# Kernel optimization log

Hardware: AMD Instinct MI355X
Metric: run time of the kernel (lower is better)

Reference implementation:

```python
import jax, jax.numpy as jnp
import numpy as np
from itertools import product

N = 65536
G = 128          # voxel grid side
K = 27           # 3^3 kernel offsets
C_IN, C_HID, C_OUT = 3, 256, 128
EPS = 1e-5


def _build_neighbors():
    rng = np.random.default_rng(0)
    keys = np.sort(rng.choice(G ** 3, size=N, replace=False))
    coords = np.stack(np.unravel_index(keys, (G, G, G)), axis=-1)  # [N,3]
    offs = np.array(list(product([-1, 0, 1], repeat=3)), dtype=np.int64)  # [27,3]
    nc = coords[:, None, :] + offs[None, :, :]                       # [N,27,3]
    inb = ((nc >= 0) & (nc < G)).all(-1)
    nk = nc[..., 0] * G * G + nc[..., 1] * G + nc[..., 2]
    pos = np.clip(np.searchsorted(keys, np.clip(nk, 0, G ** 3 - 1)), 0, N - 1)
    found = inb & (keys[pos] == nk)
    idx = np.where(found, pos, 0).astype(np.int32)
    return idx, found


def setup_inputs() -> dict:
    key = jax.random.key(0)
    ks = jax.random.split(key, 12)
    idx, mask = _build_neighbors()
    s_in = 1.0 / np.sqrt(K * C_IN)
    s_h = 1.0 / np.sqrt(K * C_HID)
    return {
        "feats": jax.random.normal(ks[0], (N, C_IN), jnp.float32),
        "w_in": jax.random.normal(ks[1], (K, C_IN, C_HID), jnp.float32) * s_in,
        "g_in": jnp.ones((C_HID,), jnp.float32),
        "b_in": jnp.zeros((C_HID,), jnp.float32),
        "w_res": jax.random.normal(ks[2], (4, 2, K, C_HID, C_HID), jnp.float32) * s_h,
        "g_res": jnp.ones((4, 2, C_HID), jnp.float32),
        "b_res": jnp.zeros((4, 2, C_HID), jnp.float32),
        "w_out": jax.random.normal(ks[3], (C_HID, C_OUT), jnp.float32) / np.sqrt(C_HID),
        "nbr_idx": jnp.asarray(idx),
        "nbr_mask": jnp.asarray(mask),
    }


def sparse_conv(feats, W, idx, mask):
    # feats [N,Cin], W [K,Cin,Cout], idx/mask [N,K] -> gather-GEMM-scatter per offset
    def step(acc, xs):
        w_k, i_k, m_k = xs  # [Cin,Cout], [N], [N]
        g = feats[i_k] * m_k[:, None]
        return acc + g @ w_k, None
    init = jnp.zeros((feats.shape[0], W.shape[-1]), feats.dtype)
    out, _ = jax.lax.scan(step, init, (W, idx.T, mask.T.astype(feats.dtype)))
    return out


def bn(x, g, b):
    mu = x.mean(0)
    var = x.var(0)
    return (x - mu) * jax.lax.rsqrt(var + EPS) * g + b


def reference(feats, w_in, g_in, b_in, w_res, g_res, b_res, w_out, nbr_idx, nbr_mask):
    h = jax.nn.relu(bn(sparse_conv(feats, w_in, nbr_idx, nbr_mask), g_in, b_in))
    for i in range(4):  # 4 MinkowskiResBlocks
        r = jax.nn.relu(bn(sparse_conv(h, w_res[i, 0], nbr_idx, nbr_mask), g_res[i, 0], b_res[i, 0]))
        r = bn(sparse_conv(r, w_res[i, 1], nbr_idx, nbr_mask), g_res[i, 1], b_res[i, 1])
        h = jax.nn.relu(r + h)
    return h @ w_out  # kernel_size=1 output conv == pointwise linear
```

## Files before the change

kernel.cpp:

```cpp
#include <hip/hip_runtime.h>
#include <hip/hip_bf16.h>


#define NPTS 65536
#define CHID 256
#define CAP  4096
#define LBLK 256

typedef __bf16 bf16x8 __attribute__((ext_vector_type(8)));
typedef float  f32x4  __attribute__((ext_vector_type(4)));
typedef unsigned short u16x8 __attribute__((ext_vector_type(8)));

__device__ __forceinline__ float bf2f(unsigned short u) {
    union { float f; unsigned v; } x; x.v = ((unsigned)u) << 16; return x.f;
}
__device__ __forceinline__ unsigned short f2bf(float f) {
    union { float f; unsigned v; } x; x.f = f;
    unsigned r = x.v + 0x7fffu + ((x.v >> 16) & 1u);
    return (unsigned short)(r >> 16);
}

__device__ __forceinline__ void gload16(const void* g, void* l) {
    __builtin_amdgcn_global_load_lds(
        (const __attribute__((address_space(1))) void*)g,
        (__attribute__((address_space(3))) void*)l, 16, 0, 0);
}

__device__ __forceinline__ bool mk(const void* mask, int mflag, size_t i) {
    if (mflag) return ((const unsigned char*)mask)[i] != 0;
    return ((const int*)mask)[i] != 0;
}

__global__ void detect_mask(const unsigned char* __restrict__ m, int* __restrict__ flag) {
    int t = blockIdx.x * 256 + threadIdx.x;
    int any = 0;
    for (int i = t; i < 262144; i += 64 * 256)
        if ((i & 3) && m[i]) any = 1;
    if (any) atomicOr(flag, 1);
}

__global__ void pack_w(const float* __restrict__ w, unsigned short* __restrict__ wp) {
    __shared__ float tile[64][65];
    int m   = blockIdx.x;
    int tci = (blockIdx.y >> 2) * 64;
    int tco = (blockIdx.y & 3) * 64;
    const float* src = w + (size_t)m * 65536;
    unsigned short* dst = wp + (size_t)m * 65536;
    int t = threadIdx.x, c = t & 63, rg = t >> 6;
    for (int r = rg; r < 64; r += 4)
        tile[r][c] = src[(size_t)(tci + r) * 256 + tco + c];
    __syncthreads();
    for (int r = rg; r < 64; r += 4)
        dst[(size_t)(tco + r) * 256 + tci + c] = f2bf(tile[c][r]);
}

__global__ void pack_wout(const float* __restrict__ w, unsigned short* __restrict__ wp) {
    __shared__ float tile[64][65];
    int tco = blockIdx.x * 64, tci = blockIdx.y * 64;
    int t = threadIdx.x, c = t & 63, rg = t >> 6;
    for (int r = rg; r < 64; r += 4)
        tile[r][c] = w[(size_t)(tci + r) * 128 + tco + c];
    __syncthreads();
    for (int r = rg; r < 64; r += 4)
        wp[(size_t)(tco + r) * 256 + tci + c] = f2bf(tile[c][r]);
}

__global__ void pack_win(const float* __restrict__ w, unsigned short* __restrict__ wp) {
    __shared__ float tile[64][65];
    int cot = blockIdx.x * 64, kkt = blockIdx.y * 64;
    int t = threadIdx.x, c = t & 63, rg = t >> 6;
    for (int r = rg; r < 64; r += 4) {
        int kk = kkt + r;
        tile[r][c] = (kk < 81) ? w[(size_t)kk * 256 + cot + c] : 0.f;
    }
    __syncthreads();
    for (int r = rg; r < 64; r += 4)
        wp[(size_t)(cot + r) * 128 + kkt + c] = f2bf(tile[c][r]);
}

__global__ void count_lists(const void* __restrict__ mask, const int* __restrict__ mflagp,
                            int* __restrict__ blkcnt ) {
    int mflag = *mflagp;
    int tid = threadIdx.x, lane = tid & 63;
    int n = blockIdx.x * 256 + tid;
    __shared__ int lc[26];
    if (tid < 26) lc[tid] = 0;
    __syncthreads();
    unsigned vb = 0;
    for (int k = 0; k < 27; ++k) {
        if (k == 13) continue;
        if (mk(mask, mflag, (size_t)n * 27 + k)) vb |= 1u << k;
    }
    for (int k26 = 0; k26 < 26; ++k26) {
        int k = (k26 < 13) ? k26 : k26 + 1;
        unsigned long long b = __ballot((vb >> k) & 1);
        if (lane == 0) atomicAdd(&lc[k26], __popcll(b));
    }
    __syncthreads();
    if (tid < 26) blkcnt[tid * LBLK + blockIdx.x] = lc[tid];
}

__global__ void scan_lists(const int* __restrict__ blkcnt, int* __restrict__ bases,
                           int* __restrict__ cnt) {
    int t = threadIdx.x;
    if (t < 26) {
        int s = 0;
        for (int b = 0; b < LBLK; ++b) {
            bases[t * LBLK + b] = s;
            s += blkcnt[t * LBLK + b];
        }
        cnt[t] = s;
    }
}

__global__ void fill_lists(const int* __restrict__ idx, const void* __restrict__ mask,
                           const int* __restrict__ mflagp, const int* __restrict__ bases,
                           int* __restrict__ srcL, int* __restrict__ nbrEnt,
                           unsigned char* __restrict__ nbrCnt) {
    int mflag = *mflagp;
    int tid = threadIdx.x, lane = tid & 63, wave = tid >> 6;
    int n = blockIdx.x * 256 + tid;
    __shared__ int wcnt[4][26];
    unsigned vb = 0;
    for (int k = 0; k < 27; ++k) {
        if (k == 13) continue;
        if (mk(mask, mflag, (size_t)n * 27 + k)) vb |= 1u << k;
    }
    for (int k26 = 0; k26 < 26; ++k26) {
        int k = (k26 < 13) ? k26 : k26 + 1;
        unsigned long long b = __ballot((vb >> k) & 1);
        if (lane == 0) wcnt[wave][k26] = __popcll(b);
    }
    __syncthreads();
    int j = 0;
    for (int k26 = 0; k26 < 26; ++k26) {
        int k = (k26 < 13) ? k26 : k26 + 1;
        bool v = (vb >> k) & 1;
        unsigned long long b = __ballot(v);
        if (v) {
            int p = bases[k26 * LBLK + blockIdx.x] + __popcll(b & ((1ull << lane) - 1ull));
            for (int w = 0; w < wave; ++w) p += wcnt[w][k26];
            if (p < CAP) {
                srcL[k26 * CAP + p] = idx[(size_t)n * 27 + k];
                nbrEnt[n * 32 + j] = k26 * CAP + p;
                ++j;
            }
        }
    }
    nbrCnt[n] = (unsigned char)j;
}

__global__ __launch_bounds__(256, 2)
void convin_gemm(const float* __restrict__ feats, const unsigned short* __restrict__ win,
                 const int* __restrict__ idx, const void* __restrict__ mask,
                 const int* __restrict__ mflagp, unsigned short* __restrict__ yb) {
    __shared__ __align__(16) char A[16384];
    __shared__ __align__(16) char B[32768];
    const int mflag = *mflagp;
    const int tid = threadIdx.x, lane = tid & 63, wave = tid >> 6;
    const int m0 = blockIdx.x * 64;

    for (int i = 0; i < 4; ++i)
        *(f32x4*)&A[tid * 64 + i * 16] = f32x4{0.f, 0.f, 0.f, 0.f};
    __syncthreads();

    {
        int row = tid & 63, g = tid >> 6;
        int n = m0 + row;
        int swz = (row & 7) << 4;
        for (int k = g; k < 27; k += 4) {
            if (mk(mask, mflag, (size_t)n * 27 + k)) {
                int j = idx[(size_t)n * 27 + k];
                float f0 = feats[j * 3 + 0], f1 = feats[j * 3 + 1], f2 = feats[j * 3 + 2];
                int b0 = 2 * (3 * k + 0), b1 = b0 + 2, b2 = b0 + 4;
                *(unsigned short*)&A[row * 256 + (b0 ^ swz)] = f2bf(f0);
                *(unsigned short*)&A[row * 256 + (b1 ^ swz)] = f2bf(f1);
                *(unsigned short*)&A[row * 256 + (b2 ^ swz)] = f2bf(f2);
            }
        }
    }

    const char* wb = (const char*)win;
    f32x4 acc[4][4] = {};

    for (int ks = 0; ks < 2; ++ks) {
        __syncthreads();
        for (int i = 0; i < 8; ++i) {
            int chunk = wave * 8 + i;
            int o = chunk * 1024 + lane * 16;
            int corow = o >> 7;
            int inner = (o & 127) ^ ((corow & 7) << 4);
            gload16(wb + (size_t)corow * 256 + ks * 128 + inner, B + o);
        }
        __syncthreads();
        const int cw = wave * 64;
        for (int kk = 0; kk < 64; kk += 32) {
            int kl = kk + 8 * (lane >> 4);
            bf16x8 af[4], bfr[4];
            for (int mi = 0; mi < 4; ++mi) {
                int row = 16 * mi + (lane & 15);
                af[mi] = *(const bf16x8*)(A + row * 256 + ((ks * 128 + 2 * kl) ^ ((row & 7) << 4)));
            }
            for (int ni = 0; ni < 4; ++ni) {
                int corow = cw + 16 * ni + (lane & 15);
                bfr[ni] = *(const bf16x8*)(B + corow * 128 + ((2 * kl) ^ ((corow & 7) << 4)));
            }
            for (int mi = 0; mi < 4; ++mi)
                for (int ni = 0; ni < 4; ++ni)
                    acc[mi][ni] = __builtin_amdgcn_mfma_f32_16x16x32_bf16(af[mi], bfr[ni], acc[mi][ni], 0, 0, 0);
        }
    }

    const int cw = wave * 64;
    const int rq = 4 * (lane >> 4);
    const int colo = lane & 15;
    for (int mi = 0; mi < 4; ++mi)
        for (int ni = 0; ni < 4; ++ni) {
            int col = cw + 16 * ni + colo;
            for (int r = 0; r < 4; ++r) {
                float v = acc[mi][ni][r];
                float o = __shfl_xor(v, 1);
                if ((lane & 1) == 0) {
                    unsigned pk = (unsigned)f2bf(v) | ((unsigned)f2bf(o) << 16);
                    int row = m0 + 16 * mi + rq + r;
                    *(unsigned*)&yb[(size_t)row * CHID + col] = pk;
                }
            }
        }
}

template<bool GATHER>
__global__ __launch_bounds__(512, 1)
void conv_gemm(const unsigned short* __restrict__ hin,
               const unsigned short* __restrict__ Wp,
               unsigned short* __restrict__ yb,
               const int* __restrict__ cnt,
               const int* __restrict__ srcL) {
    __shared__ __align__(16) char lds[131072];
    __shared__ int ids_src[256];
    const int tid  = threadIdx.x;
    const int lane = tid & 63;
    const int wave = tid >> 6;
    const int wm = wave >> 2;
    const int wn = wave & 3;

    int k27 = 13, m0 = 0, k26 = 0, tile = 0, c = 0;
    if (GATHER) {
        k26 = blockIdx.x;
        k27 = (k26 < 13) ? k26 : k26 + 1;
        tile = blockIdx.y;
        c = min(cnt[k26], CAP);
        if (tile * 256 >= c) return;
        if (tid < 256) {
            int g = tile * 256 + tid;
            ids_src[tid] = (g < c) ? srcL[k26 * CAP + g] : 0;
        }
        __syncthreads();
    } else {
        m0 = blockIdx.x * 256;
    }
    const char* hbase = (const char*)hin;
    const char* wbase = (const char*)(Wp + (size_t)k27 * (CHID * CHID));

    f32x4 acc[8][4] = {};

    auto STAGE = [&](int buf, int ks) {
        const int ci0 = ks * 64;
        char* dst = lds + buf * 65536;
        #pragma unroll
        for (int i = 0; i < 8; ++i) {
            int o = (wave * 8 + i) * 1024 + lane * 16;
            const char* src;
            if (o < 32768) {
                int row = o >> 7;
                int inner = (o & 127) ^ ((row & 7) << 4);
                int grow = GATHER ? ids_src[row] : (m0 + row);
                src = hbase + (size_t)grow * 512 + ci0 * 2 + inner;
            } else {
                int bo = o - 32768;
                int corow = bo >> 7;
                int inner = (bo & 127) ^ ((corow & 7) << 4);
                src = wbase + (size_t)corow * 512 + ci0 * 2 + inner;
            }
            gload16(src, dst + o);
        }
    };

    auto COMPUTE = [&](int buf) {
        const char* A = lds + buf * 65536;
        const char* B = A + 32768;
        #pragma unroll
        for (int kk = 0; kk < 64; kk += 32) {
            int kl = kk + 8 * (lane >> 4);
            bf16x8 af[8], bfr[4];
            #pragma unroll
            for (int mi = 0; mi < 8; ++mi) {
                int row = wm * 128 + 16 * mi + (lane & 15);
                af[mi] = *(const bf16x8*)(A + row * 128 + ((2 * kl) ^ ((row & 7) << 4)));
            }
            #pragma unroll
            for (int ni = 0; ni < 4; ++ni) {
                int corow = wn * 64 + 16 * ni + (lane & 15);
                bfr[ni] = *(const bf16x8*)(B + corow * 128 + ((2 * kl) ^ ((corow & 7) << 4)));
            }
            #pragma unroll
            for (int mi = 0; mi < 8; ++mi)
                #pragma unroll
                for (int ni = 0; ni < 4; ++ni)
                    acc[mi][ni] = __builtin_amdgcn_mfma_f32_16x16x32_bf16(af[mi], bfr[ni], acc[mi][ni], 0, 0, 0);
        }
    };

    STAGE(0, 0);
    __syncthreads();
    int cur = 0;
    #pragma unroll
    for (int ks = 0; ks < 4; ++ks) {
        if (ks < 3) STAGE(cur ^ 1, ks + 1);
        COMPUTE(cur);
        __syncthreads();
        cur ^= 1;
    }

    const int rq = 4 * (lane >> 4);
    const int colo = lane & 15;
    #pragma unroll
    for (int mi = 0; mi < 8; ++mi)
        #pragma unroll
        for (int ni = 0; ni < 4; ++ni) {
            int col = wn * 64 + 16 * ni + colo;
            #pragma unroll
            for (int r = 0; r < 4; ++r) {
                float v = acc[mi][ni][r];
                float o = __shfl_xor(v, 1);
                if ((lane & 1) == 0) {
                    unsigned pk = (unsigned)f2bf(v) | ((unsigned)f2bf(o) << 16);
                    int rl = wm * 128 + 16 * mi + rq + r;
                    if (!GATHER) {
                        *(unsigned*)&yb[(size_t)(m0 + rl) * CHID + col] = pk;
                    } else {
                        int g = tile * 256 + rl;
                        if (g < c)
                            *(unsigned*)&yb[((size_t)k26 * CAP + g) * CHID + col] = pk;
                    }
                }
            }
        }
}

__global__ __launch_bounds__(256)
void combine_stats(unsigned short* __restrict__ Yb,
                   const unsigned short* __restrict__ buf,
                   const int* __restrict__ nbrEnt,
                   const unsigned char* __restrict__ nbrCnt,
                   float* __restrict__ st) {
    __shared__ float ssum[8][256];
    __shared__ float ssq[8][256];
    const int tid = threadIdx.x;
    const int grp = tid >> 5;
    const int c0  = (tid & 31) * 8;
    float s[8] = {}, s2[8] = {};
    const int row0 = blockIdx.x * 128;
    for (int it = 0; it < 16; ++it) {
        int row = row0 + it * 8 + grp;
        size_t off = (size_t)row * CHID + c0;
        u16x8 y = *(const u16x8*)&Yb[off];
        float v[8];
        #pragma unroll
        for (int q = 0; q < 8; ++q) v[q] = bf2f(y[q]);
        int cnt = nbrCnt[row];
        for (int j = 0; j < cnt; ++j) {
            int e = nbrEnt[row * 32 + j];
            u16x8 b = *(const u16x8*)&buf[(size_t)e * CHID + c0];
            #pragma unroll
            for (int q = 0; q < 8; ++q) v[q] += bf2f(b[q]);
        }
        u16x8 o;
        #pragma unroll
        for (int q = 0; q < 8; ++q) {
            o[q] = f2bf(v[q]);
            s[q] += v[q];
            s2[q] += v[q] * v[q];
        }
        *(u16x8*)&Yb[off] = o;
    }
    #pragma unroll
    for (int q = 0; q < 8; ++q) {
        ssum[grp][c0 + q] = s[q];
        ssq[grp][c0 + q]  = s2[q];
    }
    __syncthreads();
    float ts = 0.f, tq = 0.f;
    #pragma unroll
    for (int g = 0; g < 8; ++g) { ts += ssum[g][tid]; tq += ssq[g][tid]; }
    unsafeAtomicAdd(&st[tid], ts);
    unsafeAtomicAdd(&st[256 + tid], tq);
}

__global__ void bn_stats(const unsigned short* __restrict__ yb, float* __restrict__ st) {
    int t = threadIdx.x;
    int b = blockIdx.x;
    float s = 0.f, s2 = 0.f;
    size_t base = (size_t)b * 256 * CHID + t;
    for (int i = 0; i < 256; ++i) {
        float v = bf2f(yb[base + (size_t)i * CHID]);
        s += v; s2 += v * v;
    }
    unsafeAtomicAdd(&st[t], s);
    unsafeAtomicAdd(&st[256 + t], s2);
}

__global__ void bn_apply(const unsigned short* __restrict__ yb, const float* __restrict__ st,
                         const float* __restrict__ g, const float* __restrict__ b,
                         const unsigned short* __restrict__ res, unsigned short* __restrict__ hout) {
    int t = threadIdx.x;
    float mean = st[t] * (1.f / NPTS);
    float var  = st[256 + t] * (1.f / NPTS) - mean * mean;
    float rstd = rsqrtf(var + 1e-5f);
    float sc = rstd * g[t];
    float bi = b[t] - mean * sc;
    size_t row0 = (size_t)blockIdx.x * 32;
    for (int i = 0; i < 32; ++i) {
        size_t off = (row0 + i) * CHID + t;
        float v = bf2f(yb[off]) * sc + bi;
        if (res) v += bf2f(res[off]);
        v = fmaxf(v, 0.f);
        hout[off] = f2bf(v);
    }
}

__global__ __launch_bounds__(256, 2)
void gemm_out(const unsigned short* __restrict__ hin, const unsigned short* __restrict__ wop,
              float* __restrict__ out) {
    __shared__ __align__(16) char lds[16384 + 16384];
    const int tid = threadIdx.x, lane = tid & 63, wave = tid >> 6;
    const int m0 = blockIdx.x * 128;
    const char* hb = (const char*)hin;
    const char* wb = (const char*)wop;
    f32x4 acc[4][4] = {};
    for (int ks = 0; ks < 4; ++ks) {
        int ci0 = ks * 64;
        __syncthreads();
        for (int i = 0; i < 8; ++i) {
            int chunk = wave * 8 + i;
            int o = chunk * 1024 + lane * 16;
            const char* src;
            if (o < 16384) {
                int row = o >> 7;
                int k2 = (o & 127) ^ ((row & 7) << 4);
                src = hb + (size_t)(m0 + row) * 512 + ci0 * 2 + k2;
            } else {
                int bo = o - 16384;
                int corow = bo >> 7;
                int k2 = (bo & 127) ^ ((corow & 7) << 4);
                src = wb + (size_t)corow * 512 + ci0 * 2 + k2;
            }
            gload16(src, lds + chunk * 1024);
        }
        __syncthreads();
        const char* A = lds;
        const char* B = lds + 16384;
        const int wm = wave >> 1, wn = wave & 1;
        for (int kk = 0; kk < 64; kk += 32) {
            int kl = kk + 8 * (lane >> 4);
            bf16x8 af[4], bfr[4];
            for (int mi = 0; mi < 4; ++mi) {
                int row = 64 * wm + 16 * mi + (lane & 15);
                af[mi] = *(const bf16x8*)(A + row * 128 + ((2 * kl) ^ ((row & 7) << 4)));
            }
            for (int ni = 0; ni < 4; ++ni) {
                int corow = 64 * wn + 16 * ni + (lane & 15);
                bfr[ni] = *(const bf16x8*)(B + corow * 128 + ((2 * kl) ^ ((corow & 7) << 4)));
            }
            for (int mi = 0; mi < 4; ++mi)
                for (int ni = 0; ni < 4; ++ni)
                    acc[mi][ni] = __builtin_amdgcn_mfma_f32_16x16x32_bf16(af[mi], bfr[ni], acc[mi][ni], 0, 0, 0);
        }
    }
    const int wm = wave >> 1, wn = wave & 1;
    for (int mi = 0; mi < 4; ++mi)
        for (int ni = 0; ni < 4; ++ni) {
            int col = 64 * wn + 16 * ni + (lane & 15);
            for (int r = 0; r < 4; ++r) {
                int row = m0 + 64 * wm + 16 * mi + 4 * (lane >> 4) + r;
                out[(size_t)row * 128 + col] = acc[mi][ni][r];
            }
        }
}

static const size_t OFF_Y    = 0;
static const size_t OFF_HA   = OFF_Y   + (size_t)NPTS * CHID * 2;
static const size_t OFF_HR   = OFF_HA  + (size_t)NPTS * CHID * 2;
static const size_t OFF_WP   = OFF_HR  + (size_t)NPTS * CHID * 2;
static const size_t OFF_WOP  = OFF_WP  + (size_t)8 * 27 * 65536 * 2;
static const size_t OFF_WIN  = OFF_WOP + (size_t)128 * 256 * 2;
static const size_t OFF_ST   = OFF_WIN + (size_t)256 * 128 * 2;
static const size_t OFF_CNT  = OFF_ST  + 9 * 512 * 4;
static const size_t OFF_FLAG = OFF_CNT + 112;
static const size_t OFF_SRC  = OFF_CNT + 128;
static const size_t OFF_BLK  = OFF_SRC + (size_t)26 * CAP * 4;
static const size_t OFF_BAS  = OFF_BLK + (size_t)26 * LBLK * 4;
static const size_t OFF_NBE  = OFF_BAS + (size_t)26 * LBLK * 4;
static const size_t OFF_NBC  = OFF_NBE + (size_t)NPTS * 32 * 4;
static const size_t OFF_BUF  = OFF_NBC + (size_t)NPTS;

extern "C" void kernel_launch(void* const* d_in, const int* in_sizes, int n_in,
                              void* d_out, int out_size, void* d_ws, size_t ws_size,
                              hipStream_t stream) {
    const float* feats = (const float*)d_in[0];
    const float* w_in  = (const float*)d_in[1];
    const float* g_in  = (const float*)d_in[2];
    const float* b_in  = (const float*)d_in[3];
    const float* w_res = (const float*)d_in[4];
    const float* g_res = (const float*)d_in[5];
    const float* b_res = (const float*)d_in[6];
    const float* w_out = (const float*)d_in[7];
    const int*   nidx  = (const int*)d_in[8];
    const void*  nmask = (const void*)d_in[9];

    char* ws = (char*)d_ws;
    unsigned short* Yb   = (unsigned short*)(ws + OFF_Y);
    unsigned short* HA   = (unsigned short*)(ws + OFF_HA);
    unsigned short* HR   = (unsigned short*)(ws + OFF_HR);
    unsigned short* WP   = (unsigned short*)(ws + OFF_WP);
    unsigned short* WOP  = (unsigned short*)(ws + OFF_WOP);
    unsigned short* WIN  = (unsigned short*)(ws + OFF_WIN);
    float*          ST   = (float*)(ws + OFF_ST);
    int*            CNT  = (int*)(ws + OFF_CNT);
    int*            MFLG = (int*)(ws + OFF_FLAG);
    int*            SRCL = (int*)(ws + OFF_SRC);
    int*            BLKC = (int*)(ws + OFF_BLK);
    int*            BASE = (int*)(ws + OFF_BAS);
    int*            NBE  = (int*)(ws + OFF_NBE);
    unsigned char*  NBC  = (unsigned char*)(ws + OFF_NBC);
    unsigned short* BUF  = (unsigned short*)(ws + OFF_BUF);

    hipMemsetAsync(ws + OFF_ST, 0, 9 * 512 * 4 + 128, stream);

    detect_mask<<<64, 256, 0, stream>>>((const unsigned char*)nmask, MFLG);
    pack_w   <<<dim3(216, 16), 256, 0, stream>>>(w_res, WP);
    pack_wout<<<dim3(2, 4),    256, 0, stream>>>(w_out, WOP);
    pack_win <<<dim3(4, 2),    256, 0, stream>>>(w_in, WIN);

    count_lists<<<LBLK, 256, 0, stream>>>(nmask, MFLG, BLKC);
    scan_lists <<<1, 64, 0, stream>>>(BLKC, BASE, CNT);
    fill_lists <<<LBLK, 256, 0, stream>>>(nidx, nmask, MFLG, BASE, SRCL, NBE, NBC);

    convin_gemm<<<NPTS / 64, 256, 0, stream>>>(feats, WIN, nidx, nmask, MFLG, Yb);
    bn_stats<<<256, 256, 0, stream>>>(Yb, ST);
    bn_apply<<<2048, 256, 0, stream>>>(Yb, ST, g_in, b_in, nullptr, HA);

    for (int c8 = 0; c8 < 8; ++c8) {
        const unsigned short* hin = (c8 & 1) ? HR : HA;
        const unsigned short* wbase = WP + (size_t)c8 * 27 * 65536;
        float* st = ST + (size_t)(1 + c8) * 512;
        conv_gemm<false><<<NPTS / 256, 512, 0, stream>>>(hin, wbase, Yb, nullptr, nullptr);
        conv_gemm<true><<<dim3(26, CAP / 256), 512, 0, stream>>>(hin, wbase, BUF, CNT, SRCL);
        combine_stats<<<512, 256, 0, stream>>>(Yb, BUF, NBE, NBC, st);
        if (c8 & 1) {
            bn_apply<<<2048, 256, 0, stream>>>(Yb, st, g_res + c8 * 256, b_res + c8 * 256, HA, HA);
        } else {
            bn_apply<<<2048, 256, 0, stream>>>(Yb, st, g_res + c8 * 256, b_res + c8 * 256, nullptr, HR);
        }
    }

    gemm_out<<<NPTS / 128, 256, 0, stream>>>(HA, WOP, (float*)d_out);
}
```

Before: 885.4 us.

## Vectorize BN stats/apply and replace atomics with two-stage partial reduction

```diff
diff --git a/kernel.cpp b/kernel.cpp
--- a/kernel.cpp
+++ b/kernel.cpp
@@ -6,6 +6,7 @@
 #define CHID 256
 #define CAP  4096
 #define LBLK 256
+#define CBLK 2048
 
 typedef __bf16 bf16x8 __attribute__((ext_vector_type(8)));
 typedef float  f32x4  __attribute__((ext_vector_type(4)));
@@ -353,15 +354,15 @@
                    const unsigned short* __restrict__ buf,
                    const int* __restrict__ nbrEnt,
                    const unsigned char* __restrict__ nbrCnt,
-                   float* __restrict__ st) {
+                   float* __restrict__ part) {
     __shared__ float ssum[8][256];
     __shared__ float ssq[8][256];
     const int tid = threadIdx.x;
     const int grp = tid >> 5;
     const int c0  = (tid & 31) * 8;
     float s[8] = {}, s2[8] = {};
-    const int row0 = blockIdx.x * 128;
-    for (int it = 0; it < 16; ++it) {
+    const int row0 = blockIdx.x * 32;
+    for (int it = 0; it < 4; ++it) {
         int row = row0 + it * 8 + grp;
         size_t off = (size_t)row * CHID + c0;
         u16x8 y = *(const u16x8*)&Yb[off];
@@ -393,39 +394,88 @@
     float ts = 0.f, tq = 0.f;
     #pragma unroll
     for (int g = 0; g < 8; ++g) { ts += ssum[g][tid]; tq += ssq[g][tid]; }
-    unsafeAtomicAdd(&st[tid], ts);
-    unsafeAtomicAdd(&st[256 + tid], tq);
-}
-
-__global__ void bn_stats(const unsigned short* __restrict__ yb, float* __restrict__ st) {
-    int t = threadIdx.x;
-    int b = blockIdx.x;
-    float s = 0.f, s2 = 0.f;
-    size_t base = (size_t)b * 256 * CHID + t;
-    for (int i = 0; i < 256; ++i) {
-        float v = bf2f(yb[base + (size_t)i * CHID]);
-        s += v; s2 += v * v;
-    }
-    unsafeAtomicAdd(&st[t], s);
-    unsafeAtomicAdd(&st[256 + t], s2);
-}
-
-__global__ void bn_apply(const unsigned short* __restrict__ yb, const float* __restrict__ st,
-                         const float* __restrict__ g, const float* __restrict__ b,
-                         const unsigned short* __restrict__ res, unsigned short* __restrict__ hout) {
-    int t = threadIdx.x;
-    float mean = st[t] * (1.f / NPTS);
-    float var  = st[256 + t] * (1.f / NPTS) - mean * mean;
-    float rstd = rsqrtf(var + 1e-5f);
-    float sc = rstd * g[t];
-    float bi = b[t] - mean * sc;
-    size_t row0 = (size_t)blockIdx.x * 32;
-    for (int i = 0; i < 32; ++i) {
-        size_t off = (row0 + i) * CHID + t;
-        float v = bf2f(yb[off]) * sc + bi;
-        if (res) v += bf2f(res[off]);
-        v = fmaxf(v, 0.f);
-        hout[off] = f2bf(v);
+    part[(size_t)blockIdx.x * 512 + tid]       = ts;
+    part[(size_t)blockIdx.x * 512 + 256 + tid] = tq;
+}
+
+__global__ __launch_bounds__(256)
+void bn_stats_vec(const unsigned short* __restrict__ Yb, float* __restrict__ part) {
+    __shared__ float ssum[8][256];
+    __shared__ float ssq[8][256];
+    const int tid = threadIdx.x;
+    const int grp = tid >> 5;
+    const int c0  = (tid & 31) * 8;
+    float s[8] = {}, s2[8] = {};
+    const int row0 = blockIdx.x * 32;
+    for (int it = 0; it < 4; ++it) {
+        int row = row0 + it * 8 + grp;
+        u16x8 y = *(const u16x8*)&Yb[(size_t)row * CHID + c0];
+        #pragma unroll
+        for (int q = 0; q < 8; ++q) {
+            float v = bf2f(y[q]);
+            s[q] += v; s2[q] += v * v;
+        }
+    }
+    #pragma unroll
+    for (int q = 0; q < 8; ++q) {
+        ssum[grp][c0 + q] = s[q];
+        ssq[grp][c0 + q]  = s2[q];
+    }
+    __syncthreads();
+    float ts = 0.f, tq = 0.f;
+    #pragma unroll
+    for (int g = 0; g < 8; ++g) { ts += ssum[g][tid]; tq += ssq[g][tid]; }
+    part[(size_t)blockIdx.x * 512 + tid]       = ts;
+    part[(size_t)blockIdx.x * 512 + 256 + tid] = tq;
+}
+
+__global__ void reduce_stats(const float* __restrict__ part, float* __restrict__ st) {
+    int gt = blockIdx.x * 256 + threadIdx.x;
+    int c = gt & 511;
+    int chunk = gt >> 9;
+    float s = 0.f;
+    for (int i = 0; i < CBLK / 16; ++i)
+        s += part[(size_t)(chunk * (CBLK / 16) + i) * 512 + c];
+    unsafeAtomicAdd(&st[c], s);
+}
+
+__global__ __launch_bounds__(256)
+void bn_apply(const unsigned short* __restrict__ yb, const float* __restrict__ st,
+              const float* __restrict__ g, const float* __restrict__ b,
+              const unsigned short* __restrict__ res, unsigned short* __restrict__ hout) {
+    const int tid = threadIdx.x;
+    const int grp = tid >> 5;
+    const int c0  = (tid & 31) * 8;
+    float sc[8], bi[8];
+    #pragma unroll
+    for (int q = 0; q < 8; ++q) {
+        float mean = st[c0 + q] * (1.f / NPTS);
+        float var  = st[256 + c0 + q] * (1.f / NPTS) - mean * mean;
+        float rstd = rsqrtf(var + 1e-5f);
+        sc[q] = rstd * g[c0 + q];
+        bi[q] = b[c0 + q] - mean * sc[q];
+    }
+    const int row0 = blockIdx.x * 32;
+    for (int it = 0; it < 4; ++it) {
+        int row = row0 + it * 8 + grp;
+        size_t off = (size_t)row * CHID + c0;
+        u16x8 y = *(const u16x8*)&yb[off];
+        u16x8 o;
+        if (res) {
+            u16x8 rr = *(const u16x8*)&res[off];
+            #pragma unroll
+            for (int q = 0; q < 8; ++q) {
+                float v = bf2f(y[q]) * sc[q] + bi[q] + bf2f(rr[q]);
+                o[q] = f2bf(fmaxf(v, 0.f));
+            }
+        } else {
+            #pragma unroll
+            for (int q = 0; q < 8; ++q) {
+                float v = bf2f(y[q]) * sc[q] + bi[q];
+                o[q] = f2bf(fmaxf(v, 0.f));
+            }
+        }
+        *(u16x8*)&hout[off] = o;
     }
 }
 
@@ -502,7 +552,8 @@
 static const size_t OFF_BAS  = OFF_BLK + (size_t)26 * LBLK * 4;
 static const size_t OFF_NBE  = OFF_BAS + (size_t)26 * LBLK * 4;
 static const size_t OFF_NBC  = OFF_NBE + (size_t)NPTS * 32 * 4;
-static const size_t OFF_BUF  = OFF_NBC + (size_t)NPTS;
+static const size_t OFF_PART = OFF_NBC + (size_t)NPTS;
+static const size_t OFF_BUF  = OFF_PART + (size_t)CBLK * 512 * 4;
 
 extern "C" void kernel_launch(void* const* d_in, const int* in_sizes, int n_in,
                               void* d_out, int out_size, void* d_ws, size_t ws_size,
@@ -533,6 +584,7 @@
     int*            BASE = (int*)(ws + OFF_BAS);
     int*            NBE  = (int*)(ws + OFF_NBE);
     unsigned char*  NBC  = (unsigned char*)(ws + OFF_NBC);
+    float*          PART = (float*)(ws + OFF_PART);
     unsigned short* BUF  = (unsigned short*)(ws + OFF_BUF);
 
     hipMemsetAsync(ws + OFF_ST, 0, 9 * 512 * 4 + 128, stream);
@@ -547,8 +599,9 @@
     fill_lists <<<LBLK, 256, 0, stream>>>(nidx, nmask, MFLG, BASE, SRCL, NBE, NBC);
 
     convin_gemm<<<NPTS / 64, 256, 0, stream>>>(feats, WIN, nidx, nmask, MFLG, Yb);
-    bn_stats<<<256, 256, 0, stream>>>(Yb, ST);
-    bn_apply<<<2048, 256, 0, stream>>>(Yb, ST, g_in, b_in, nullptr, HA);
+    bn_stats_vec<<<CBLK, 256, 0, stream>>>(Yb, PART);
+    reduce_stats<<<32, 256, 0, stream>>>(PART, ST);
+    bn_apply<<<CBLK, 256, 0, stream>>>(Yb, ST, g_in, b_in, nullptr, HA);
 
     for (int c8 = 0; c8 < 8; ++c8) {
         const unsigned short* hin = (c8 & 1) ? HR : HA;
@@ -556,11 +609,12 @@
         float* st = ST + (size_t)(1 + c8) * 512;
         conv_gemm<false><<<NPTS / 256, 512, 0, stream>>>(hin, wbase, Yb, nullptr, nullptr);
         conv_gemm<true><<<dim3(26, CAP / 256), 512, 0, stream>>>(hin, wbase, BUF, CNT, SRCL);
-        combine_stats<<<512, 256, 0, stream>>>(Yb, BUF, NBE, NBC, st);
+        combine_stats<<<CBLK, 256, 0, stream>>>(Yb, BUF, NBE, NBC, PART);
+        reduce_stats<<<32, 256, 0, stream>>>(PART, st);
         if (c8 & 1) {
-            bn_apply<<<2048, 256, 0, stream>>>(Yb, st, g_res + c8 * 256, b_res + c8 * 256, HA, HA);
+            bn_apply<<<CBLK, 256, 0, stream>>>(Yb, st, g_res + c8 * 256, b_res + c8 * 256, HA, HA);
         } else {
-            bn_apply<<<2048, 256, 0, stream>>>(Yb, st, g_res + c8 * 256, b_res + c8 * 256, nullptr, HR);
+            bn_apply<<<CBLK, 256, 0, stream>>>(Yb, st, g_res + c8 * 256, b_res + c8 * 256, nullptr, HR);
         }
     }
 
```

Result: faster. 788.0 us (-11.0%).
